# Kernel optimization log

Hardware: AMD Instinct MI355X
Metric: run time of the kernel (lower is better)

## Reference

```python
import jax, jax.numpy as jnp
import numpy as np

EPS_BN = 1e-5
EPS_NORM = 1e-12


def _l2norm_c(x):
    # F.normalize over channel dim (dim=1) of [n, d, h, w]
    n = jnp.sqrt(jnp.sum(x * x, axis=1, keepdims=True))
    return x / jnp.maximum(n, EPS_NORM)


def setup_inputs() -> dict:
    key = jax.random.key(0)
    ks = jax.random.split(key, 8)
    g, p, d, h, w = 64, 64, 512, 24, 8
    hw = h * w
    return {
        "gal_fea": jax.random.normal(ks[0], (g, d, h, w), dtype=jnp.float32),
        "prob_fea": jax.random.normal(ks[1], (p, d, h, w), dtype=jnp.float32),
        "bn_weight": jax.random.uniform(ks[2], (1,), dtype=jnp.float32) + 0.5,
        "bn_bias": jax.random.uniform(ks[3], (1,), dtype=jnp.float32) - 0.5,
        "bn_mean": jnp.zeros((1,), dtype=jnp.float32),
        "bn_var": jnp.ones((1,), dtype=jnp.float32),
        "fc_weight": jax.random.normal(ks[4], (1, 2 * hw), dtype=jnp.float32) * 0.05,
        "fc_bias": jax.random.normal(ks[5], (1,), dtype=jnp.float32) * 0.05,
        "lbn_weight": jax.random.uniform(ks[6], (1,), dtype=jnp.float32) + 0.5,
        "lbn_bias": jax.random.uniform(ks[7], (1,), dtype=jnp.float32) - 0.5,
        "lbn_mean": jnp.zeros((1,), dtype=jnp.float32),
        "lbn_var": jnp.ones((1,), dtype=jnp.float32),
    }


def reference(gal_fea, prob_fea, bn_weight, bn_bias, bn_mean, bn_var,
              fc_weight, fc_bias, lbn_weight, lbn_bias, lbn_mean, lbn_var):
    g, d, h, w = gal_fea.shape
    p = prob_fea.shape[0]
    hw = h * w

    # L2-normalize over channels, flatten spatial dims
    gal = _l2norm_c(gal_fea).reshape(g, d, hw)              # [g, d, j]
    ker = _l2norm_c(prob_fea).transpose(0, 2, 3, 1).reshape(p, hw, d)  # [p, i, d]

    # cosine-similarity cross-correlation: s[g,p,i,j] = <probe pos i, gallery pos j>
    s = jnp.einsum('pid,gdj->gpij', ker, gal)               # [g, p, hw, hw]

    # dual spatial max-pool: max over probe positions, max over gallery positions
    score = jnp.concatenate([s.max(axis=2), s.max(axis=3)], axis=-1)  # [g, p, 2*hw]

    # eval-mode BatchNorm1d(1): scalar affine broadcast over all elements
    score = (score - bn_mean) / jnp.sqrt(bn_var + EPS_BN) * bn_weight + bn_bias

    # fc: Linear(2*hw, 1)
    score = jnp.einsum('gpk,ok->gpo', score, fc_weight)[..., 0] + fc_bias[0]  # [g, p]

    # eval-mode logit BatchNorm1d(1): scalar affine
    score = (score - lbn_mean) / jnp.sqrt(lbn_var + EPS_BN) * lbn_weight + lbn_bias

    return jax.nn.sigmoid(score / 10.0)
```

## Files before the change

kernel.cpp:

```cpp
#include <hip/hip_runtime.h>

#define HW 192
#define DD 512
#define GG 64
#define PP 64
#define SLAB 98304

typedef __attribute__((ext_vector_type(4))) int intx4;

__device__ __forceinline__ unsigned int pk4(float a, float b, float c, float d) {
  int qa = (int)rintf(a), qb = (int)rintf(b), qc = (int)rintf(c), qd = (int)rintf(d);
  return (unsigned)(qa & 255) | ((unsigned)(qb & 255) << 8) |
         ((unsigned)(qc & 255) << 16) | ((unsigned)(qd & 255) << 24);
}

__global__ __launch_bounds__(512, 2) void norm_kernel(
    const float* __restrict__ gal, const float* __restrict__ prob,
    unsigned char* __restrict__ ws) {
  int b = blockIdx.x;
  int s = b / 12;
  int q = b - s * 12;
  const float* in = (s < GG) ? (gal + (size_t)s * DD * HW)
                             : (prob + (size_t)(s - GG) * DD * HW);
  unsigned char* out = ws + (size_t)s * SLAB;
  int pos0 = q * 16;
  int t = threadIdx.x;

  __shared__ float T[16][524];
  __shared__ float sqa[128][17];
  __shared__ float sq2[16][17];
  __shared__ float scl[16];

  {
    int cq = t >> 2;
    int quad = t & 3;
    float p0 = 0.f, p1 = 0.f, p2 = 0.f, p3 = 0.f;
#pragma unroll
    for (int cb = 0; cb < 4; ++cb) {
      int c = cb * 128 + cq;
      const float4 v = *(const float4*)(in + (size_t)c * HW + pos0 + quad * 4);
      T[quad * 4 + 0][c] = v.x;
      T[quad * 4 + 1][c] = v.y;
      T[quad * 4 + 2][c] = v.z;
      T[quad * 4 + 3][c] = v.w;
      p0 += v.x * v.x; p1 += v.y * v.y; p2 += v.z * v.z; p3 += v.w * v.w;
    }
    sqa[cq][quad * 4 + 0] = p0;
    sqa[cq][quad * 4 + 1] = p1;
    sqa[cq][quad * 4 + 2] = p2;
    sqa[cq][quad * 4 + 3] = p3;
  }
  __syncthreads();
  if (t < 256) {
    int g2 = t >> 4, pos = t & 15;
    float v = 0.f;
#pragma unroll
    for (int r = 0; r < 8; ++r) v += sqa[g2 * 8 + r][pos];
    sq2[g2][pos] = v;
  }
  __syncthreads();
  if (t < 16) {
    float v = 0.f;
#pragma unroll
    for (int r = 0; r < 16; ++r) v += sq2[r][t];
    scl[t] = 1.f / fmaxf(sqrtf(v), 1e-12f);
  }
  __syncthreads();

  {
    int kb2 = t >> 6;
    int lane = t & 63;
    int l4 = lane >> 4;
    int pos = lane & 15;
    float sc = scl[pos] * 127.f;
    int base = kb2 * 64 + l4 * 16;
    const float4 r0 = *(const float4*)&T[pos][base + 0];
    const float4 r1 = *(const float4*)&T[pos][base + 4];
    const float4 r2 = *(const float4*)&T[pos][base + 8];
    const float4 r3 = *(const float4*)&T[pos][base + 12];
    uint4 u;
    u.x = pk4(r0.x * sc, r0.y * sc, r0.z * sc, r0.w * sc);
    u.y = pk4(r1.x * sc, r1.y * sc, r1.z * sc, r1.w * sc);
    u.z = pk4(r2.x * sc, r2.y * sc, r2.z * sc, r2.w * sc);
    u.w = pk4(r3.x * sc, r3.y * sc, r3.z * sc, r3.w * sc);
    *(uint4*)(out + (size_t)kb2 * 12288 + (size_t)q * 1024 + (size_t)lane * 16) = u;
  }
}

__global__ __launch_bounds__(256, 2) void qaconv_gemm(
    const unsigned char* __restrict__ ws, const float* __restrict__ fcw,
    const float* __restrict__ bnw, const float* __restrict__ bnb,
    const float* __restrict__ bnm, const float* __restrict__ bnv,
    const float* __restrict__ fcb, const float* __restrict__ lw,
    const float* __restrict__ lb, const float* __restrict__ lm,
    const float* __restrict__ lv, float* __restrict__ out) {
  int bid0 = blockIdx.x;
  int bid = ((bid0 & 7) << 9) + (bid0 >> 3);
  int sb = bid >> 6, li = bid & 63;
  int g = ((sb >> 3) << 3) + (li >> 3);
  int p = ((sb & 7) << 3) + (li & 7);
  const unsigned char* Bsrc = ws + (size_t)g * SLAB;
  const unsigned char* Asrc = ws + (size_t)(GG + p) * SLAB;

  __shared__ float colpart[2][HW];
  __shared__ float rowpart[2][HW];
  __shared__ float redbuf[4][2];

  int tid = threadIdx.x;
  int lane = tid & 63;
  int wave = tid >> 6;
  int wi = wave >> 1, wj = wave & 1;
  int l15 = lane & 15, l4 = lane >> 4;

  intx4 acc[6][6];
#pragma unroll
  for (int a = 0; a < 6; ++a)
#pragma unroll
    for (int c = 0; c < 6; ++c) acc[a][c] = (intx4){0, 0, 0, 0};

  const unsigned char* aP = Asrc + (size_t)(wi * 6) * 1024 + (size_t)lane * 16;
  const unsigned char* bP = Bsrc + (size_t)(wj * 6) * 1024 + (size_t)lane * 16;

#define LOADF(AD, BD, KB)                                                 \
  do {                                                                    \
    _Pragma("unroll") for (int it_ = 0; it_ < 6; ++it_) {                 \
      AD[it_] = *(const intx4*)(aP + (size_t)(KB)*12288 + it_ * 1024);    \
      BD[it_] = *(const intx4*)(bP + (size_t)(KB)*12288 + it_ * 1024);    \
    }                                                                     \
  } while (0)

#define MFMAB(AD, BD)                                                     \
  do {                                                                    \
    _Pragma("unroll") for (int jt_ = 0; jt_ < 6; ++jt_) {                 \
      intx4 bb = BD[jt_];                                                 \
      _Pragma("unroll") for (int it_ = 0; it_ < 6; ++it_)                 \
          acc[it_][jt_] = __builtin_amdgcn_mfma_i32_16x16x64_i8(          \
              AD[it_], bb, acc[it_][jt_], 0, 0, 0);                       \
    }                                                                     \
  } while (0)

  intx4 aC[6], bC[6], aN[6], bN[6];
  LOADF(aC, bC, 0);
#pragma unroll 1
  for (int kb2 = 0; kb2 < 8; kb2 += 2) {
    LOADF(aN, bN, kb2 + 1);
    MFMAB(aC, bC);
    if (kb2 < 6) LOADF(aC, bC, kb2 + 2);
    MFMAB(aN, bN);
  }
#undef LOADF
#undef MFMAB

  const float inv = 1.f / 16129.f;
  int cm[6];
  int rm[6][4];
#pragma unroll
  for (int jt = 0; jt < 6; ++jt) cm[jt] = -2147483647;
#pragma unroll
  for (int it = 0; it < 6; ++it)
#pragma unroll
    for (int r = 0; r < 4; ++r) rm[it][r] = -2147483647;
#pragma unroll
  for (int it = 0; it < 6; ++it)
#pragma unroll
    for (int jt = 0; jt < 6; ++jt)
#pragma unroll
      for (int r = 0; r < 4; ++r) {
        int v = acc[it][jt][r];
        cm[jt] = max(cm[jt], v);
        rm[it][r] = max(rm[it][r], v);
      }

#pragma unroll
  for (int jt = 0; jt < 6; ++jt) {
    int v = cm[jt];
    v = max(v, __shfl_xor(v, 16, 64));
    v = max(v, __shfl_xor(v, 32, 64));
    if (lane < 16) colpart[wi][wj * 96 + jt * 16 + lane] = (float)v * inv;
  }
#pragma unroll
  for (int it = 0; it < 6; ++it)
#pragma unroll
    for (int r = 0; r < 4; ++r) {
      int v = rm[it][r];
      v = max(v, __shfl_xor(v, 1, 64));
      v = max(v, __shfl_xor(v, 2, 64));
      v = max(v, __shfl_xor(v, 4, 64));
      v = max(v, __shfl_xor(v, 8, 64));
      if (l15 == 0) rowpart[wj][wi * 96 + it * 16 + l4 * 4 + r] = (float)v * inv;
    }
  __syncthreads();

  float part = 0.f, wpart = 0.f;
  if (tid < HW) {
    float cmax = fmaxf(colpart[0][tid], colpart[1][tid]);
    float rmax = fmaxf(rowpart[0][tid], rowpart[1][tid]);
    float w1 = fcw[tid], w2 = fcw[HW + tid];
    part = cmax * w1 + rmax * w2;
    wpart = w1 + w2;
  }
#pragma unroll
  for (int off = 32; off > 0; off >>= 1) {
    part += __shfl_down(part, off, 64);
    wpart += __shfl_down(wpart, off, 64);
  }
  if (lane == 0) { redbuf[wave][0] = part; redbuf[wave][1] = wpart; }
  __syncthreads();
  if (tid == 0) {
    float s = redbuf[0][0] + redbuf[1][0] + redbuf[2][0] + redbuf[3][0];
    float wsum = redbuf[0][1] + redbuf[1][1] + redbuf[2][1] + redbuf[3][1];
    float bnA = bnw[0] * rsqrtf(bnv[0] + 1e-5f);
    float bnB = bnb[0] - bnm[0] * bnA;
    float sc = bnA * s + bnB * wsum + fcb[0];
    float lA = lw[0] * rsqrtf(lv[0] + 1e-5f);
    sc = (sc - lm[0]) * lA + lb[0];
    out[g * PP + p] = 1.f / (1.f + __expf(-sc * 0.1f));
  }
}

extern "C" void kernel_launch(void* const* d_in, const int* in_sizes, int n_in,
                              void* d_out, int out_size, void* d_ws, size_t ws_size,
                              hipStream_t stream) {
  const float* gal  = (const float*)d_in[0];
  const float* prob = (const float*)d_in[1];
  const float* bnw  = (const float*)d_in[2];
  const float* bnb  = (const float*)d_in[3];
  const float* bnm  = (const float*)d_in[4];
  const float* bnv  = (const float*)d_in[5];
  const float* fcw  = (const float*)d_in[6];
  const float* fcb  = (const float*)d_in[7];
  const float* lw   = (const float*)d_in[8];
  const float* lb   = (const float*)d_in[9];
  const float* lm   = (const float*)d_in[10];
  const float* lv   = (const float*)d_in[11];
  unsigned char* ws = (unsigned char*)d_ws;
  float* out = (float*)d_out;

  hipLaunchKernelGGL(norm_kernel, dim3(1536), dim3(512), 0, stream, gal, prob, ws);
  hipLaunchKernelGGL(qaconv_gemm, dim3(GG * PP), dim3(256), 0, stream, ws, fcw,
                     bnw, bnb, bnm, bnv, fcb, lw, lb, lm, lv, out);
}
```

Before: 196.7 us.

## Stage int8 GEMM operands through double-buffered LDS via direct global-to-LDS loads

Each wave previously loaded its A and B fragments straight from global memory into registers, so every A and B tile was fetched by two waves. Now each of the four waves issues async global_load_lds copies for one quarter of the block's A/B tiles into a double-buffered 48KB shared buffer, and all waves then read their fragments from LDS. This halves global/L2 traffic per block and frees registers, at the cost of a block-wide barrier every k-step and less prefetch depth than the earlier register double-buffering. The reduction scratch arrays are aliased onto the same shared buffer after the loop.

Measured after the change: 212.1 us. +7.8%, slower.

```diff
diff --git a/kernel.cpp b/kernel.cpp
--- a/kernel.cpp
+++ b/kernel.cpp
@@ -87,6 +87,11 @@
   }
 }
 
+#define GLOAD_LDS16(gp, lp)                                              \
+  __builtin_amdgcn_global_load_lds(                                      \
+      (const __attribute__((address_space(1))) unsigned int*)(gp),       \
+      (__attribute__((address_space(3))) unsigned int*)(lp), 16, 0, 0)
+
 __global__ __launch_bounds__(256, 2) void qaconv_gemm(
     const unsigned char* __restrict__ ws, const float* __restrict__ fcw,
     const float* __restrict__ bnw, const float* __restrict__ bnb,
@@ -102,9 +107,7 @@
   const unsigned char* Bsrc = ws + (size_t)g * SLAB;
   const unsigned char* Asrc = ws + (size_t)(GG + p) * SLAB;
 
-  __shared__ float colpart[2][HW];
-  __shared__ float rowpart[2][HW];
-  __shared__ float redbuf[4][2];
+  __shared__ unsigned char sbuf[2][24576];
 
   int tid = threadIdx.x;
   int lane = tid & 63;
@@ -118,38 +121,47 @@
 #pragma unroll
     for (int c = 0; c < 6; ++c) acc[a][c] = (intx4){0, 0, 0, 0};
 
-  const unsigned char* aP = Asrc + (size_t)(wi * 6) * 1024 + (size_t)lane * 16;
-  const unsigned char* bP = Bsrc + (size_t)(wj * 6) * 1024 + (size_t)lane * 16;
-
-#define LOADF(AD, BD, KB)                                                 \
+  const unsigned char* stgsrc =
+      ((wave < 2) ? Asrc : Bsrc) + (size_t)((wave & 1) * 6) * 1024 +
+      (size_t)lane * 16;
+  int fbase = wave * 6;
+
+#define STAGE(BUF, KB)                                                    \
   do {                                                                    \
-    _Pragma("unroll") for (int it_ = 0; it_ < 6; ++it_) {                 \
-      AD[it_] = *(const intx4*)(aP + (size_t)(KB)*12288 + it_ * 1024);    \
-      BD[it_] = *(const intx4*)(bP + (size_t)(KB)*12288 + it_ * 1024);    \
+    const unsigned char* s_ = stgsrc + (size_t)(KB)*12288;                \
+    _Pragma("unroll") for (int i_ = 0; i_ < 6; ++i_) {                    \
+      GLOAD_LDS16(s_ + i_ * 1024, &sbuf[BUF][(fbase + i_) * 1024]);       \
     }                                                                     \
   } while (0)
 
-#define MFMAB(AD, BD)                                                     \
-  do {                                                                    \
-    _Pragma("unroll") for (int jt_ = 0; jt_ < 6; ++jt_) {                 \
-      intx4 bb = BD[jt_];                                                 \
-      _Pragma("unroll") for (int it_ = 0; it_ < 6; ++it_)                 \
-          acc[it_][jt_] = __builtin_amdgcn_mfma_i32_16x16x64_i8(          \
-              AD[it_], bb, acc[it_][jt_], 0, 0, 0);                       \
-    }                                                                     \
-  } while (0)
-
-  intx4 aC[6], bC[6], aN[6], bN[6];
-  LOADF(aC, bC, 0);
+  STAGE(0, 0);
 #pragma unroll 1
-  for (int kb2 = 0; kb2 < 8; kb2 += 2) {
-    LOADF(aN, bN, kb2 + 1);
-    MFMAB(aC, bC);
-    if (kb2 < 6) LOADF(aC, bC, kb2 + 2);
-    MFMAB(aN, bN);
-  }
-#undef LOADF
-#undef MFMAB
+  for (int kb = 0; kb < 8; ++kb) {
+    __syncthreads();
+    if (kb < 7) STAGE((kb + 1) & 1, kb + 1);
+    const unsigned char* cb = &sbuf[kb & 1][lane * 16];
+    intx4 a[6], b[6];
+#pragma unroll
+    for (int i = 0; i < 6; ++i) {
+      a[i] = *(const intx4*)(cb + (wi * 6 + i) * 1024);
+      b[i] = *(const intx4*)(cb + (12 + wj * 6 + i) * 1024);
+    }
+#pragma unroll
+    for (int jt = 0; jt < 6; ++jt) {
+      intx4 bb = b[jt];
+#pragma unroll
+      for (int it = 0; it < 6; ++it)
+        acc[it][jt] = __builtin_amdgcn_mfma_i32_16x16x64_i8(a[it], bb,
+                                                            acc[it][jt], 0, 0, 0);
+    }
+  }
+#undef STAGE
+
+  __syncthreads();
+
+  float (*colpart)[HW] = (float (*)[HW]) & sbuf[0][0];
+  float (*rowpart)[HW] = (float (*)[HW]) & sbuf[0][1536];
+  float (*redbuf)[2] = (float (*)[2]) & sbuf[0][3072];
 
   const float inv = 1.f / 16129.f;
   int cm[6];
```
